# Performance work log

Hardware: AMD Instinct MI355X
Metric: run time of the kernel (lower is better)

The kernel has to match this reference:

```python
import jax, jax.numpy as jnp
import numpy as np
import math

NEG_INF = float('-inf')

def setup_inputs() -> dict:
    key = jax.random.key(0)
    ks = jax.random.split(key, 5)
    B, T, C = 8, 2048, 1024
    x = jax.random.normal(ks[0], (B, T, C), dtype=jnp.float32)
    W_kqv = jax.random.normal(ks[1], (C, 3 * C), dtype=jnp.float32) * (1.0 / math.sqrt(C))
    b_kqv = jax.random.normal(ks[2], (3 * C,), dtype=jnp.float32) * 0.02
    W_proj = jax.random.normal(ks[3], (C, C), dtype=jnp.float32) * (1.0 / math.sqrt(C))
    b_proj = jax.random.normal(ks[4], (C,), dtype=jnp.float32) * 0.02
    return {"x": x, "W_kqv": W_kqv, "b_kqv": b_kqv, "W_proj": W_proj, "b_proj": b_proj}

def reference(x, W_kqv, b_kqv, W_proj, b_proj):
    B, T, C = x.shape
    kqv = x @ W_kqv + b_kqv                      # [B,T,3C]
    k, q, v = jnp.split(kqv, 3, axis=-1)         # split order k, q, v (as in source)
    # NOTE: source scales by 1/sqrt(k.size(-1)) AFTER transposing k -> 1/sqrt(T)
    scale = 1.0 / math.sqrt(T)
    scores = jnp.einsum('btc,bsc->bts', q, k) * scale  # [B,T,T]
    mask = jnp.tril(jnp.ones((T, T), dtype=bool))[None, None]  # [1,1,T,T]
    # broadcasting mirrors torch masked_fill: [B,T,T] vs [1,1,T,T] -> [1,B,T,T]
    scores = jnp.where(mask, scores, NEG_INF)    # [1,B,T,T]
    att = jax.nn.softmax(scores, axis=-1)        # [1,B,T,T]
    out = jnp.matmul(att, v)                     # [1,B,T,C]
    out = out @ W_proj + b_proj                  # [1,B,T,C]
    return out
```

## Files before the change

kernel.cpp:

```cpp
#include <hip/hip_runtime.h>

typedef unsigned short u16;
typedef __attribute__((ext_vector_type(8))) __bf16 bf16x8;
typedef __attribute__((ext_vector_type(8))) unsigned short u16x8;
typedef __attribute__((ext_vector_type(4))) unsigned short u16x4;
typedef __attribute__((ext_vector_type(4))) float f32x4;

#define BM 256
#define BN 256
#define BK 64

__device__ __forceinline__ float bf2f(u16 x) {
  union { unsigned int u; float f; } un;
  un.u = ((unsigned int)x) << 16;
  return un.f;
}

__device__ __forceinline__ u16 f2bf(float f) {
  union { float f; unsigned int u; } un;
  un.f = f;
  unsigned int r = un.u + 0x7fffu + ((un.u >> 16) & 1u);
  return (u16)(r >> 16);
}

__device__ __forceinline__ void cstore(u16* p, float v)   { *p = f2bf(v); }
__device__ __forceinline__ void cstore(float* p, float v) { *p = v; }

__device__ __forceinline__ void async_ld16(const u16* g, u16* l) {
  __builtin_amdgcn_global_load_lds(
      (const __attribute__((address_space(1))) unsigned int*)g,
      (__attribute__((address_space(3))) unsigned int*)l, 16, 0, 0);
}

__device__ __forceinline__ bf16x8 ldfrag(const u16* p) {
  union { u16x8 u; bf16x8 b; } c;
  c.u = *(const u16x8*)p;
  return c.b;
}

__global__ __launch_bounds__(256)
void f32_to_bf16(const float* __restrict__ s, u16* __restrict__ d)
{
  const int i = blockIdx.x * 256 + threadIdx.x;
  const float4 v = ((const float4*)s)[i];
  u16x4 o;
  o.x = f2bf(v.x); o.y = f2bf(v.y); o.z = f2bf(v.z); o.w = f2bf(v.w);
  ((u16x4*)d)[i] = o;
}

__global__ __launch_bounds__(256)
void transpose_f2b(const float* __restrict__ src, int sld,
                   u16* __restrict__ dst, int dld)
{
  __shared__ float tile[32][33];
  const int c0 = blockIdx.x * 32;
  const int r0 = blockIdx.y * 32;
  const int tx = threadIdx.x;
  const int ty = threadIdx.y;
#pragma unroll
  for (int i = ty; i < 32; i += 8)
    tile[i][tx] = src[(long long)(r0 + i) * sld + c0 + tx];
  __syncthreads();
#pragma unroll
  for (int i = ty; i < 32; i += 8)
    dst[(long long)(c0 + i) * dld + r0 + tx] = f2bf(tile[tx][i]);
}

__global__ __launch_bounds__(256)
void transpose_bf16(const u16* __restrict__ src, int sld, long long sbs,
                    u16* __restrict__ dst, int dld, long long dbs)
{
  src += (long long)blockIdx.z * sbs;
  dst += (long long)blockIdx.z * dbs;
  __shared__ u16 tile[32][33];
  const int c0 = blockIdx.x * 32;
  const int r0 = blockIdx.y * 32;
  const int tx = threadIdx.x;
  const int ty = threadIdx.y;
#pragma unroll
  for (int i = ty; i < 32; i += 8)
    tile[i][tx] = src[(long long)(r0 + i) * sld + c0 + tx];
  __syncthreads();
#pragma unroll
  for (int i = ty; i < 32; i += 8)
    dst[(long long)(c0 + i) * dld + r0 + tx] = tile[tx][i];
}

template <typename OT>
__global__ __launch_bounds__(512, 2)
void gemm_nt(const u16* __restrict__ A, int lda, long long sA,
             const u16* __restrict__ Bt, int ldb, long long sB,
             OT* __restrict__ Cp, int ldc, long long sC,
             int K, const float* __restrict__ bias, float scale, int mode)
{
  int bx = blockIdx.x, by = blockIdx.y;
  const int bz = blockIdx.z;
  if (mode == 3) { bx = blockIdx.y; by = blockIdx.x; }
  if (mode == 1 && by > bx) return;
  A  += (long long)bz * sA;
  Bt += (long long)bz * sB;
  Cp += (long long)bz * sC;
  int kEnd = K;
  if (mode == 2) { int ke = (bx + 1) * BM; kEnd = ke < K ? ke : K; }

  __shared__ __align__(16) u16 As[2][BM * BK];
  __shared__ __align__(16) u16 Bs[2][BM * BK];

  const int tid  = threadIdx.x;
  const int wave = tid >> 6;
  const int lane = tid & 63;
  const int l16  = lane & 15;
  const int quad = lane >> 4;
  const int wm = wave >> 2;
  const int wn = wave & 3;

  const int sk0 = ((quad    ) ^ (l16 & 7)) * 8;
  const int sk1 = ((quad + 4) ^ (l16 & 7)) * 8;
  const int arow = wm * 128 + l16;
  const int brow = wn * 64  + l16;

  const int srow8 = lane >> 3;
  const int sx    = ((lane & 7) ^ srow8) * 8;

  const int f0 = (wave < 4) ? (2 * wave) : (16 + 2 * (wave - 4));
  const int aCh[4] = { f0, f0 + 1, f0 + 8, f0 + 9 };

  const u16* Bgp[4];
#pragma unroll
  for (int p = 0; p < 4; ++p)
    Bgp[p] = Bt + (long long)(by * BN + (4 * wave + p) * 8 + srow8) * ldb + sx;
  const u16* Agp[4];
#pragma unroll
  for (int q = 0; q < 4; ++q)
    Agp[q] = A + (long long)(bx * BM + aCh[q] * 8 + srow8) * lda + sx;

  f32x4 zero4;
  zero4.x = zero4.y = zero4.z = zero4.w = 0.0f;
  f32x4 acc[8][4];
#pragma unroll
  for (int i = 0; i < 8; ++i)
#pragma unroll
    for (int j = 0; j < 4; ++j) acc[i][j] = zero4;

  const int nt = kEnd / BK;

#pragma unroll
  for (int p = 0; p < 4; ++p) async_ld16(Bgp[p], &Bs[0][(4 * wave + p) * 512]);
#pragma unroll
  for (int q = 0; q < 4; ++q) async_ld16(Agp[q], &As[0][aCh[q] * 512]);
  asm volatile("s_waitcnt vmcnt(2)" ::: "memory");
  __builtin_amdgcn_s_barrier();

  for (int j = 0; j < nt; ++j) {
    const int cur = j & 1;
    const int nxt = cur ^ 1;
    const bool pf = (j + 1 < nt);
    const int ko = (j + 1) * BK;

    bf16x8 bv0[4], bv1[4], av[4];

#pragma unroll
    for (int n = 0; n < 4; ++n) bv0[n] = ldfrag(&Bs[cur][(brow + n * 16) * BK + sk0]);
#pragma unroll
    for (int i = 0; i < 4; ++i) av[i]  = ldfrag(&As[cur][(arow + i * 16) * BK + sk0]);
    if (pf) {
      async_ld16(Bgp[0] + ko, &Bs[nxt][(4 * wave + 0) * 512]);
      async_ld16(Bgp[1] + ko, &Bs[nxt][(4 * wave + 1) * 512]);
    }
    asm volatile("" ::: "memory");
    __builtin_amdgcn_s_barrier();
    __builtin_amdgcn_s_setprio(1);
#pragma unroll
    for (int i = 0; i < 4; ++i)
#pragma unroll
      for (int n = 0; n < 4; ++n)
        acc[i][n] = __builtin_amdgcn_mfma_f32_16x16x32_bf16(av[i], bv0[n], acc[i][n], 0, 0, 0);
    __builtin_amdgcn_s_setprio(0);
    asm volatile("" ::: "memory");
    __builtin_amdgcn_s_barrier();

#pragma unroll
    for (int n = 0; n < 4; ++n) bv1[n] = ldfrag(&Bs[cur][(brow + n * 16) * BK + sk1]);
#pragma unroll
    for (int i = 0; i < 4; ++i) av[i]  = ldfrag(&As[cur][(arow + i * 16) * BK + sk1]);
    if (pf) {
      async_ld16(Bgp[2] + ko, &Bs[nxt][(4 * wave + 2) * 512]);
      async_ld16(Bgp[3] + ko, &Bs[nxt][(4 * wave + 3) * 512]);
    }
    asm volatile("" ::: "memory");
    __builtin_amdgcn_s_barrier();
    __builtin_amdgcn_s_setprio(1);
#pragma unroll
    for (int i = 0; i < 4; ++i)
#pragma unroll
      for (int n = 0; n < 4; ++n)
        acc[i][n] = __builtin_amdgcn_mfma_f32_16x16x32_bf16(av[i], bv1[n], acc[i][n], 0, 0, 0);
    __builtin_amdgcn_s_setprio(0);
    if (pf) asm volatile("s_waitcnt vmcnt(4)" ::: "memory");
    else    asm volatile("s_waitcnt vmcnt(0)" ::: "memory");
    __builtin_amdgcn_s_barrier();

#pragma unroll
    for (int i = 0; i < 4; ++i) av[i] = ldfrag(&As[cur][(arow + (i + 4) * 16) * BK + sk0]);
    if (pf) {
      async_ld16(Agp[0] + ko, &As[nxt][aCh[0] * 512]);
      async_ld16(Agp[1] + ko, &As[nxt][aCh[1] * 512]);
    }
    asm volatile("" ::: "memory");
    __builtin_amdgcn_s_barrier();
    __builtin_amdgcn_s_setprio(1);
#pragma unroll
    for (int i = 0; i < 4; ++i)
#pragma unroll
      for (int n = 0; n < 4; ++n)
        acc[i + 4][n] = __builtin_amdgcn_mfma_f32_16x16x32_bf16(av[i], bv0[n], acc[i + 4][n], 0, 0, 0);
    __builtin_amdgcn_s_setprio(0);
    asm volatile("" ::: "memory");
    __builtin_amdgcn_s_barrier();

#pragma unroll
    for (int i = 0; i < 4; ++i) av[i] = ldfrag(&As[cur][(arow + (i + 4) * 16) * BK + sk1]);
    if (pf) {
      async_ld16(Agp[2] + ko, &As[nxt][aCh[2] * 512]);
      async_ld16(Agp[3] + ko, &As[nxt][aCh[3] * 512]);
    }
    asm volatile("" ::: "memory");
    __builtin_amdgcn_s_barrier();
    __builtin_amdgcn_s_setprio(1);
#pragma unroll
    for (int i = 0; i < 4; ++i)
#pragma unroll
      for (int n = 0; n < 4; ++n)
        acc[i + 4][n] = __builtin_amdgcn_mfma_f32_16x16x32_bf16(av[i], bv1[n], acc[i + 4][n], 0, 0, 0);
    __builtin_amdgcn_s_setprio(0);
    if (pf) asm volatile("s_waitcnt vmcnt(2)" ::: "memory");
    __builtin_amdgcn_s_barrier();
  }

  const long long row0 = (long long)bx * BM + wm * 128 + quad * 4;
  const int col0 = by * BN + wn * 64 + l16;
#pragma unroll
  for (int j = 0; j < 4; ++j) {
    const int col = col0 + j * 16;
    const float bval = bias ? bias[col] : 0.0f;
#pragma unroll
    for (int i = 0; i < 8; ++i) {
#pragma unroll
      for (int r = 0; r < 4; ++r) {
        const long long row = row0 + i * 16 + r;
        cstore(&Cp[row * ldc + col], acc[i][j][r] * scale + bval);
      }
    }
  }
}

__global__ __launch_bounds__(256)
void softmax_causal(u16* __restrict__ sc, int T)
{
  const int row = blockIdx.x;
  const int t = row & (T - 1);
  u16* p = sc + (long long)row * T;
  const int L  = t + 1;
  const int Lw = ((t >> 8) + 1) << 8;
  const int tid = threadIdx.x;
  const int lane = tid & 63;
  const int wave = tid >> 6;
  const int base = tid * 8;

  const u16x8 in = *(const u16x8*)(p + base);
  float v[8];
  float m = -1e30f;
#pragma unroll
  for (int e = 0; e < 8; ++e) {
    const float f = bf2f(in[e]);
    v[e] = (base + e < L) ? f : -1e30f;
    m = fmaxf(m, v[e]);
  }
#pragma unroll
  for (int o = 32; o > 0; o >>= 1) m = fmaxf(m, __shfl_xor(m, o, 64));
  __shared__ float redm[4], reds[4];
  if (lane == 0) redm[wave] = m;
  __syncthreads();
  m = fmaxf(fmaxf(redm[0], redm[1]), fmaxf(redm[2], redm[3]));

  float s = 0.0f;
#pragma unroll
  for (int e = 0; e < 8; ++e) {
    const float ex = __expf(v[e] - m);
    v[e] = (base + e < L) ? ex : 0.0f;
    s += v[e];
  }
#pragma unroll
  for (int o = 32; o > 0; o >>= 1) s += __shfl_xor(s, o, 64);
  if (lane == 0) reds[wave] = s;
  __syncthreads();
  s = reds[0] + reds[1] + reds[2] + reds[3];
  const float inv = 1.0f / s;

  if (base < Lw) {
    u16x8 o8;
#pragma unroll
    for (int e = 0; e < 8; ++e) o8[e] = f2bf(v[e] * inv);
    *(u16x8*)(p + base) = o8;
  }
}

extern "C" void kernel_launch(void* const* d_in, const int* in_sizes, int n_in,
                              void* d_out, int out_size, void* d_ws, size_t ws_size,
                              hipStream_t stream)
{
  (void)in_sizes; (void)n_in; (void)out_size; (void)ws_size;
  const int B = 8, T = 2048, C = 1024;
  const int M = B * T;
  const int C3 = 3 * C;

  const float* x     = (const float*)d_in[0];
  const float* Wkqv  = (const float*)d_in[1];
  const float* bkqv  = (const float*)d_in[2];
  const float* Wproj = (const float*)d_in[3];
  const float* bproj = (const float*)d_in[4];
  float* out = (float*)d_out;

  char* w = (char*)d_ws;
  u16* xb     = (u16*)w; w += (size_t)M * C * 2;
  u16* WkqvT  = (u16*)w; w += (size_t)C3 * C * 2;
  u16* WprojT = (u16*)w; w += (size_t)C * C * 2;
  u16* kqv    = (u16*)w; w += (size_t)M * C3 * 2;
  u16* vT     = (u16*)w; w += (size_t)B * C * T * 2;
  u16* sc     = (u16*)w; w += (size_t)B * T * T * 2;
  u16* ao     = xb;

  dim3 tb(32, 8);

  f32_to_bf16<<<(M * C) / 1024, 256, 0, stream>>>(x, xb);

  transpose_f2b<<<dim3(C3 / 32, C / 32, 1), tb, 0, stream>>>(Wkqv, C3, WkqvT, C);
  transpose_f2b<<<dim3(C / 32, C / 32, 1), tb, 0, stream>>>(Wproj, C, WprojT, C);

  gemm_nt<u16><<<dim3(C3 / BN, M / BM, 1), 512, 0, stream>>>(
      xb, C, 0, WkqvT, C, 0, kqv, C3, 0, C, bkqv, 1.0f, 3);

  transpose_bf16<<<dim3(C / 32, T / 32, B), tb, 0, stream>>>(
      kqv + 2 * C, C3, (long long)T * C3, vT, T, (long long)C * T);

  gemm_nt<u16><<<dim3(T / BM, T / BN, B), 512, 0, stream>>>(
      kqv + C, C3, (long long)T * C3, kqv, C3, (long long)T * C3,
      sc, T, (long long)T * T, C, nullptr, 0.022097086912079608f, 1);

  softmax_causal<<<B * T, 256, 0, stream>>>(sc, T);

  gemm_nt<u16><<<dim3(T / BM, C / BN, B), 512, 0, stream>>>(
      sc, T, (long long)T * T, vT, T, (long long)C * T,
      ao, C, (long long)T * C, T, nullptr, 1.0f, 2);

  gemm_nt<float><<<dim3(M / BM, C / BN, 1), 512, 0, stream>>>(
      ao, C, 0, WprojT, C, 0, out, C, 0, C, bproj, 1.0f, 0);
}
```

Baseline: 502.9 us.

## Fuse V transpose into QKV GEMM epilogue, preload LDS fragments, skip masked softmax loads

```diff
diff --git a/kernel.cpp b/kernel.cpp
--- a/kernel.cpp
+++ b/kernel.cpp
@@ -66,32 +66,13 @@
     dst[(long long)(c0 + i) * dld + r0 + tx] = f2bf(tile[tx][i]);
 }
 
-__global__ __launch_bounds__(256)
-void transpose_bf16(const u16* __restrict__ src, int sld, long long sbs,
-                    u16* __restrict__ dst, int dld, long long dbs)
-{
-  src += (long long)blockIdx.z * sbs;
-  dst += (long long)blockIdx.z * dbs;
-  __shared__ u16 tile[32][33];
-  const int c0 = blockIdx.x * 32;
-  const int r0 = blockIdx.y * 32;
-  const int tx = threadIdx.x;
-  const int ty = threadIdx.y;
-#pragma unroll
-  for (int i = ty; i < 32; i += 8)
-    tile[i][tx] = src[(long long)(r0 + i) * sld + c0 + tx];
-  __syncthreads();
-#pragma unroll
-  for (int i = ty; i < 32; i += 8)
-    dst[(long long)(c0 + i) * dld + r0 + tx] = tile[tx][i];
-}
-
 template <typename OT>
 __global__ __launch_bounds__(512, 2)
 void gemm_nt(const u16* __restrict__ A, int lda, long long sA,
              const u16* __restrict__ Bt, int ldb, long long sB,
              OT* __restrict__ Cp, int ldc, long long sC,
-             int K, const float* __restrict__ bias, float scale, int mode)
+             int K, const float* __restrict__ bias, float scale, int mode,
+             u16* __restrict__ vdst)
 {
   int bx = blockIdx.x, by = blockIdx.y;
   const int bz = blockIdx.z;
@@ -157,12 +138,16 @@
     const bool pf = (j + 1 < nt);
     const int ko = (j + 1) * BK;
 
-    bf16x8 bv0[4], bv1[4], av[4];
+    bf16x8 bv0[4], bv1[4], av0[4], av1[4];
 
 #pragma unroll
     for (int n = 0; n < 4; ++n) bv0[n] = ldfrag(&Bs[cur][(brow + n * 16) * BK + sk0]);
 #pragma unroll
-    for (int i = 0; i < 4; ++i) av[i]  = ldfrag(&As[cur][(arow + i * 16) * BK + sk0]);
+    for (int i = 0; i < 4; ++i) av0[i] = ldfrag(&As[cur][(arow + i * 16) * BK + sk0]);
+#pragma unroll
+    for (int n = 0; n < 4; ++n) bv1[n] = ldfrag(&Bs[cur][(brow + n * 16) * BK + sk1]);
+#pragma unroll
+    for (int i = 0; i < 4; ++i) av1[i] = ldfrag(&As[cur][(arow + i * 16) * BK + sk1]);
     if (pf) {
       async_ld16(Bgp[0] + ko, &Bs[nxt][(4 * wave + 0) * 512]);
       async_ld16(Bgp[1] + ko, &Bs[nxt][(4 * wave + 1) * 512]);
@@ -174,15 +159,11 @@
     for (int i = 0; i < 4; ++i)
 #pragma unroll
       for (int n = 0; n < 4; ++n)
-        acc[i][n] = __builtin_amdgcn_mfma_f32_16x16x32_bf16(av[i], bv0[n], acc[i][n], 0, 0, 0);
+        acc[i][n] = __builtin_amdgcn_mfma_f32_16x16x32_bf16(av0[i], bv0[n], acc[i][n], 0, 0, 0);
     __builtin_amdgcn_s_setprio(0);
     asm volatile("" ::: "memory");
     __builtin_amdgcn_s_barrier();
 
-#pragma unroll
-    for (int n = 0; n < 4; ++n) bv1[n] = ldfrag(&Bs[cur][(brow + n * 16) * BK + sk1]);
-#pragma unroll
-    for (int i = 0; i < 4; ++i) av[i]  = ldfrag(&As[cur][(arow + i * 16) * BK + sk1]);
     if (pf) {
       async_ld16(Bgp[2] + ko, &Bs[nxt][(4 * wave + 2) * 512]);
       async_ld16(Bgp[3] + ko, &Bs[nxt][(4 * wave + 3) * 512]);
@@ -194,14 +175,16 @@
     for (int i = 0; i < 4; ++i)
 #pragma unroll
       for (int n = 0; n < 4; ++n)
-        acc[i][n] = __builtin_amdgcn_mfma_f32_16x16x32_bf16(av[i], bv1[n], acc[i][n], 0, 0, 0);
+        acc[i][n] = __builtin_amdgcn_mfma_f32_16x16x32_bf16(av1[i], bv1[n], acc[i][n], 0, 0, 0);
     __builtin_amdgcn_s_setprio(0);
     if (pf) asm volatile("s_waitcnt vmcnt(4)" ::: "memory");
     else    asm volatile("s_waitcnt vmcnt(0)" ::: "memory");
     __builtin_amdgcn_s_barrier();
 
 #pragma unroll
-    for (int i = 0; i < 4; ++i) av[i] = ldfrag(&As[cur][(arow + (i + 4) * 16) * BK + sk0]);
+    for (int i = 0; i < 4; ++i) av0[i] = ldfrag(&As[cur][(arow + (i + 4) * 16) * BK + sk0]);
+#pragma unroll
+    for (int i = 0; i < 4; ++i) av1[i] = ldfrag(&As[cur][(arow + (i + 4) * 16) * BK + sk1]);
     if (pf) {
       async_ld16(Agp[0] + ko, &As[nxt][aCh[0] * 512]);
       async_ld16(Agp[1] + ko, &As[nxt][aCh[1] * 512]);
@@ -213,13 +196,11 @@
     for (int i = 0; i < 4; ++i)
 #pragma unroll
       for (int n = 0; n < 4; ++n)
-        acc[i + 4][n] = __builtin_amdgcn_mfma_f32_16x16x32_bf16(av[i], bv0[n], acc[i + 4][n], 0, 0, 0);
+        acc[i + 4][n] = __builtin_amdgcn_mfma_f32_16x16x32_bf16(av0[i], bv0[n], acc[i + 4][n], 0, 0, 0);
     __builtin_amdgcn_s_setprio(0);
     asm volatile("" ::: "memory");
     __builtin_amdgcn_s_barrier();
 
-#pragma unroll
-    for (int i = 0; i < 4; ++i) av[i] = ldfrag(&As[cur][(arow + (i + 4) * 16) * BK + sk1]);
     if (pf) {
       async_ld16(Agp[2] + ko, &As[nxt][aCh[2] * 512]);
       async_ld16(Agp[3] + ko, &As[nxt][aCh[3] * 512]);
@@ -231,24 +212,44 @@
     for (int i = 0; i < 4; ++i)
 #pragma unroll
       for (int n = 0; n < 4; ++n)
-        acc[i + 4][n] = __builtin_amdgcn_mfma_f32_16x16x32_bf16(av[i], bv1[n], acc[i + 4][n], 0, 0, 0);
+        acc[i + 4][n] = __builtin_amdgcn_mfma_f32_16x16x32_bf16(av1[i], bv1[n], acc[i + 4][n], 0, 0, 0);
     __builtin_amdgcn_s_setprio(0);
     if (pf) asm volatile("s_waitcnt vmcnt(2)" ::: "memory");
     __builtin_amdgcn_s_barrier();
   }
 
-  const long long row0 = (long long)bx * BM + wm * 128 + quad * 4;
-  const int col0 = by * BN + wn * 64 + l16;
-#pragma unroll
-  for (int j = 0; j < 4; ++j) {
-    const int col = col0 + j * 16;
-    const float bval = bias ? bias[col] : 0.0f;
-#pragma unroll
-    for (int i = 0; i < 8; ++i) {
-#pragma unroll
-      for (int r = 0; r < 4; ++r) {
-        const long long row = row0 + i * 16 + r;
-        cstore(&Cp[row * ldc + col], acc[i][j][r] * scale + bval);
+  const bool isv = (vdst != nullptr) && (by * BN >= 2048);
+  if (isv) {
+    const int b  = bx >> 3;
+    const int t0 = (bx & 7) * BM + wm * 128 + quad * 4;
+    u16* vb = vdst + (long long)b * 1024 * 2048;
+    const int vc0 = by * BN - 2048 + wn * 64 + l16;
+#pragma unroll
+    for (int j = 0; j < 4; ++j) {
+      const int vc = vc0 + j * 16;
+      const float bval = bias ? bias[2048 + vc] : 0.0f;
+#pragma unroll
+      for (int i = 0; i < 8; ++i) {
+        u16x4 o;
+#pragma unroll
+        for (int r = 0; r < 4; ++r) o[r] = f2bf(acc[i][j][r] * scale + bval);
+        *(u16x4*)(vb + (long long)vc * 2048 + t0 + i * 16) = o;
+      }
+    }
+  } else {
+    const long long row0 = (long long)bx * BM + wm * 128 + quad * 4;
+    const int col0 = by * BN + wn * 64 + l16;
+#pragma unroll
+    for (int j = 0; j < 4; ++j) {
+      const int col = col0 + j * 16;
+      const float bval = bias ? bias[col] : 0.0f;
+#pragma unroll
+      for (int i = 0; i < 8; ++i) {
+#pragma unroll
+        for (int r = 0; r < 4; ++r) {
+          const long long row = row0 + i * 16 + r;
+          cstore(&Cp[row * ldc + col], acc[i][j][r] * scale + bval);
+        }
       }
     }
   }
@@ -267,14 +268,19 @@
   const int wave = tid >> 6;
   const int base = tid * 8;
 
-  const u16x8 in = *(const u16x8*)(p + base);
   float v[8];
   float m = -1e30f;
-#pragma unroll
-  for (int e = 0; e < 8; ++e) {
-    const float f = bf2f(in[e]);
-    v[e] = (base + e < L) ? f : -1e30f;
-    m = fmaxf(m, v[e]);
+  if (base < Lw) {
+    const u16x8 in = *(const u16x8*)(p + base);
+#pragma unroll
+    for (int e = 0; e < 8; ++e) {
+      const float f = bf2f(in[e]);
+      v[e] = (base + e < L) ? f : -1e30f;
+      m = fmaxf(m, v[e]);
+    }
+  } else {
+#pragma unroll
+    for (int e = 0; e < 8; ++e) v[e] = -1e30f;
   }
 #pragma unroll
   for (int o = 32; o > 0; o >>= 1) m = fmaxf(m, __shfl_xor(m, o, 64));
@@ -338,21 +344,18 @@
   transpose_f2b<<<dim3(C / 32, C / 32, 1), tb, 0, stream>>>(Wproj, C, WprojT, C);
 
   gemm_nt<u16><<<dim3(C3 / BN, M / BM, 1), 512, 0, stream>>>(
-      xb, C, 0, WkqvT, C, 0, kqv, C3, 0, C, bkqv, 1.0f, 3);
-
-  transpose_bf16<<<dim3(C / 32, T / 32, B), tb, 0, stream>>>(
-      kqv + 2 * C, C3, (long long)T * C3, vT, T, (long long)C * T);
+      xb, C, 0, WkqvT, C, 0, kqv, C3, 0, C, bkqv, 1.0f, 3, vT);
 
   gemm_nt<u16><<<dim3(T / BM, T / BN, B), 512, 0, stream>>>(
       kqv + C, C3, (long long)T * C3, kqv, C3, (long long)T * C3,
-      sc, T, (long long)T * T, C, nullptr, 0.022097086912079608f, 1);
+      sc, T, (long long)T * T, C, nullptr, 0.022097086912079608f, 1, nullptr);
 
   softmax_causal<<<B * T, 256, 0, stream>>>(sc, T);
 
   gemm_nt<u16><<<dim3(T / BM, C / BN, B), 512, 0, stream>>>(
       sc, T, (long long)T * T, vT, T, (long long)C * T,
-      ao, C, (long long)T * C, T, nullptr, 1.0f, 2);
+      ao, C, (long long)T * C, T, nullptr, 1.0f, 2, nullptr);
 
   gemm_nt<float><<<dim3(M / BM, C / BN, 1), 512, 0, stream>>>(
-      ao, C, 0, WprojT, C, 0, out, C, 0, C, bproj, 1.0f, 0);
-}
+      ao, C, 0, WprojT, C, 0, out, C, 0, C, bproj, 1.0f, 0, nullptr);
+}
```

New measurement: 468.3 us. 1.07x faster.
